# Kernel optimization log

Hardware: AMD Instinct MI355X
Metric: run time of the kernel (lower is better)

## Reference

```python
import jax, jax.numpy as jnp
import numpy as np

HEAD_SIZE = 64
EMBED_DIM = 1024
SEQ_LEN = 4096
BATCH = 4


def setup_inputs() -> dict:
    key = jax.random.key(0)
    kx, kk, kq, kv = jax.random.split(key, 4)
    x = jax.random.normal(kx, (BATCH, SEQ_LEN, EMBED_DIM), dtype=jnp.float32)
    # nn.Linear(embedding_dim, head_size, bias=False): weight [head_size, embed];
    # store transposed [embed, head_size] so projection is x @ W.
    scale = 1.0 / np.sqrt(EMBED_DIM)
    Wk = jax.random.uniform(kk, (EMBED_DIM, HEAD_SIZE), jnp.float32, -scale, scale)
    Wq = jax.random.uniform(kq, (EMBED_DIM, HEAD_SIZE), jnp.float32, -scale, scale)
    Wv = jax.random.uniform(kv, (EMBED_DIM, HEAD_SIZE), jnp.float32, -scale, scale)
    return {"x": x, "Wk": Wk, "Wq": Wq, "Wv": Wv}


def reference(x, Wk, Wq, Wv):
    B, T, C = x.shape
    k = x @ Wk  # [B, T, H]
    q = x @ Wq  # [B, T, H]
    v = x @ Wv  # [B, T, H]
    H = k.shape[-1]
    s = jnp.einsum('bth,bsh->bts', q, k) * (H ** -0.5)  # [B, T, T]
    causal = jnp.tril(jnp.ones((T, T), dtype=bool))
    s = jnp.where(causal, s, -jnp.inf)
    a = jax.nn.softmax(s, axis=-1)  # dropout p=0.0 -> identity
    z = jnp.einsum('bts,bsh->bth', a, v)  # [B, T, H]
    return z
```

## Files before the change

### kernel.cpp

```cpp
#include <hip/hip_runtime.h>

#define SEQ 4096
#define EMB 1024
#define HS 64

typedef __attribute__((ext_vector_type(8))) short bf16x8;
typedef __attribute__((ext_vector_type(4))) float f32x4;

__device__ __forceinline__ unsigned short f2b(float f) {
    union { float f; unsigned u; } v; v.f = f;
    unsigned r = v.u + 0x7fffu + ((v.u >> 16) & 1u);
    return (unsigned short)(r >> 16);
}
__device__ __forceinline__ float b2f(unsigned short h) {
    union { unsigned u; float f; } v; v.u = ((unsigned)h) << 16;
    return v.f;
}
template <typename T>
__device__ __forceinline__ void gll16(const T* g, void* l) {
    __builtin_amdgcn_global_load_lds(
        (const __attribute__((address_space(1))) unsigned int*)(g),
        (__attribute__((address_space(3))) unsigned int*)(l), 16, 0, 0);
}

__global__ __launch_bounds__(256) void wt_kernel(const float* __restrict__ Wq,
                                                 const float* __restrict__ Wk,
                                                 const float* __restrict__ Wv,
                                                 unsigned short* __restrict__ Wt) {
    int id = blockIdx.x * 256 + threadIdx.x;
    int mat = id >> 16;
    int rem = id & 65535;
    int k = rem >> 6;
    int n = rem & 63;
    const float* W = (mat == 0) ? Wq : (mat == 1) ? Wk : Wv;
    float scale = (mat == 0) ? 0.125f * 1.44269504f : 1.0f;
    Wt[(mat * HS + n) * EMB + k] = f2b(W[k * HS + n] * scale);
}

__global__ __launch_bounds__(256, 2) void proj_kernel(const float* __restrict__ x,
                                                      const unsigned short* __restrict__ Wt,
                                                      unsigned short* __restrict__ Qb,
                                                      unsigned short* __restrict__ Kb,
                                                      unsigned short* __restrict__ Vt) {
    __shared__ float xf[2][32 * 64];
    __shared__ unsigned short wb[2][192 * 64];
    const int tid = threadIdx.x;
    const int wave = tid >> 6, lane = tid & 63;
    const int col = lane & 15, quad = lane >> 4;
    const int m0 = blockIdx.x * 32;
    const int b = m0 >> 12, t0 = m0 & 4095;

    const int xr_in = lane >> 4;
    const int xc = lane & 15;
    const int wr_in = lane >> 3;
    const int wc = lane & 7;

    f32x4 acc[2][3];
    #pragma unroll
    for (int i = 0; i < 2; i++)
        #pragma unroll
        for (int j = 0; j < 3; j++) acc[i][j] = (f32x4){0.f, 0.f, 0.f, 0.f};

    auto stage = [&](int k0, int bufi) {
        #pragma unroll
        for (int t = 0; t < 2; t++) {
            int R = (wave + t * 4) * 4;
            int row = R + xr_in;
            gll16(x + (size_t)(m0 + row) * EMB + k0 + ((xc ^ (row & 15)) << 2),
                  &xf[bufi][R * 64]);
        }
        #pragma unroll
        for (int t = 0; t < 6; t++) {
            int R = (wave * 6 + t) * 8;
            int row = R + wr_in;
            gll16(Wt + (size_t)row * EMB + k0 + ((wc ^ (row & 7)) << 3),
                  &wb[bufi][R * 64]);
        }
    };

    stage(0, 0);
    int buf = 0;
    #pragma unroll 1
    for (int k0 = 0; k0 < EMB; k0 += 64) {
        __syncthreads();
        if (k0 + 64 < EMB) stage(k0 + 64, buf ^ 1);
        #pragma unroll
        for (int kc = 0; kc < 2; kc++) {
            const int q2 = quad + kc * 4;
            bf16x8 af[2], bfr[3];
            #pragma unroll
            for (int mt = 0; mt < 2; mt++) {
                int rr = mt * 16 + col;
                float4 lo = *(const float4*)&xf[buf][rr * 64 + (((2 * q2) ^ col) << 2)];
                float4 hi = *(const float4*)&xf[buf][rr * 64 + (((2 * q2 + 1) ^ col) << 2)];
                bf16x8 a;
                a[0] = (short)f2b(lo.x); a[1] = (short)f2b(lo.y);
                a[2] = (short)f2b(lo.z); a[3] = (short)f2b(lo.w);
                a[4] = (short)f2b(hi.x); a[5] = (short)f2b(hi.y);
                a[6] = (short)f2b(hi.z); a[7] = (short)f2b(hi.w);
                af[mt] = a;
            }
            #pragma unroll
            for (int nt = 0; nt < 3; nt++) {
                int rn = wave * 48 + nt * 16 + col;
                bfr[nt] = *(const bf16x8*)&wb[buf][rn * 64 + ((q2 ^ (col & 7)) << 3)];
            }
            #pragma unroll
            for (int mt = 0; mt < 2; mt++)
                #pragma unroll
                for (int nt = 0; nt < 3; nt++)
                    acc[mt][nt] = __builtin_amdgcn_mfma_f32_16x16x32_bf16(af[mt], bfr[nt], acc[mt][nt], 0, 0, 0);
        }
        buf ^= 1;
    }

    #pragma unroll
    for (int mt = 0; mt < 2; mt++)
        #pragma unroll
        for (int nt = 0; nt < 3; nt++) {
            const int g = wave * 3 + nt;
            const int mat = g >> 2;
            const int ncol = (g & 3) * 16 + col;
            #pragma unroll
            for (int r = 0; r < 4; r++) {
                unsigned short val = f2b(acc[mt][nt][r]);
                int row = mt * 16 + quad * 4 + r;
                if (mat == 0)      Qb[(size_t)(m0 + row) * HS + ncol] = val;
                else if (mat == 1) Kb[(size_t)(m0 + row) * HS + ncol] = val;
                else               Vt[((size_t)b * HS + ncol) * SEQ + t0 + row] = val;
            }
        }
}

__global__ __launch_bounds__(512, 4) void attn_kernel(const unsigned short* __restrict__ Qb,
                                                      const unsigned short* __restrict__ Kb,
                                                      const unsigned short* __restrict__ Vt,
                                                      unsigned short* __restrict__ Opart,
                                                      float* __restrict__ Lpart) {
    __shared__ unsigned short Kl[2][64 * 64];
    __shared__ unsigned short Vl[2][64 * 64];
    __shared__ unsigned short P_lds[8][16 * 72];
    const int tid = threadIdx.x;
    const int wave = tid >> 6, lane = tid & 63;
    const int col = lane & 15, quad = lane >> 4;
    const int bid = blockIdx.x;
    const int g = 101 - (bid >> 2);
    const int b = bid & 3;
    int T = 0, accp = 0;
    for (;;) { int np = (T + 6) / 6; if (accp + np > g) break; accp += np; T++; }
    const int piece = g - accp;
    const int q0 = T << 7;
    const int s_beg = piece * 12;
    const int s_end = min(s_beg + 12, 2 * T + 2);

    const unsigned short* Kp = Kb + ((size_t)(b << 12)) * HS;
    const unsigned short* Vp = Vt + (size_t)b * HS * SEQ;

    bf16x8 qf[2];
    #pragma unroll
    for (int c = 0; c < 2; c++)
        qf[c] = *(const bf16x8*)(Qb + ((size_t)(b << 12) + q0 + wave * 16 + col) * HS + quad * 8 + c * 32);

    f32x4 o[4];
    float l[4];
    #pragma unroll
    for (int ct = 0; ct < 4; ct++) o[ct] = (f32x4){0.f, 0.f, 0.f, 0.f};
    #pragma unroll
    for (int r = 0; r < 4; r++) l[r] = 0.f;

    const int r_in = lane >> 3;
    const int ch = lane & 7;

    auto stage = [&](int s, int bufi) {
        const int kv0 = s << 6;
        int R = wave * 8;
        int row = R + r_in;
        gll16(Kp + (size_t)(kv0 + row) * HS + ((ch ^ (row & 7)) << 3), &Kl[bufi][R * 64]);
        gll16(Vp + (size_t)row * SEQ + kv0 + ((ch ^ (row & 7)) << 3), &Vl[bufi][R * 64]);
    };

    stage(s_beg, 0);
    int buf = 0;
    const int rgb = q0 + wave * 16 + quad * 4;
    unsigned short* Pl = P_lds[wave];

    #pragma unroll 1
    for (int s = s_beg; s < s_end; s++) {
        __syncthreads();
        if (s + 1 < s_end) stage(s + 1, buf ^ 1);
        const int kv0 = s << 6;

        f32x4 sacc[4];
        #pragma unroll
        for (int ct = 0; ct < 4; ct++) sacc[ct] = (f32x4){0.f, 0.f, 0.f, 0.f};
        #pragma unroll
        for (int ct = 0; ct < 4; ct++) {
            int n = ct * 16 + col;
            #pragma unroll
            for (int kc = 0; kc < 2; kc++) {
                bf16x8 kf = *(const bf16x8*)&Kl[buf][n * 64 + (((kc * 4 + quad) ^ (col & 7)) << 3)];
                sacc[ct] = __builtin_amdgcn_mfma_f32_16x16x32_bf16(qf[kc], kf, sacc[ct], 0, 0, 0);
            }
        }

        float p[4][4];
        #pragma unroll
        for (int ct = 0; ct < 4; ct++) {
            int cg = kv0 + ct * 16 + col;
            #pragma unroll
            for (int r = 0; r < 4; r++) {
                float e = __builtin_exp2f(sacc[ct][r]);
                e = (cg > rgb + r) ? 0.f : e;
                p[ct][r] = e;
                l[r] += e;
            }
        }

        #pragma unroll
        for (int ct = 0; ct < 4; ct++)
            #pragma unroll
            for (int r = 0; r < 4; r++)
                Pl[(quad * 4 + r) * 72 + ct * 16 + col] = f2b(p[ct][r]);
        bf16x8 pf[2];
        #pragma unroll
        for (int c = 0; c < 2; c++)
            pf[c] = *(const bf16x8*)&Pl[col * 72 + quad * 8 + c * 32];

        #pragma unroll
        for (int ct = 0; ct < 4; ct++) {
            int h = ct * 16 + col;
            #pragma unroll
            for (int kc = 0; kc < 2; kc++) {
                bf16x8 vf = *(const bf16x8*)&Vl[buf][h * 64 + (((kc * 4 + quad) ^ (col & 7)) << 3)];
                o[ct] = __builtin_amdgcn_mfma_f32_16x16x32_bf16(pf[kc], vf, o[ct], 0, 0, 0);
            }
        }
        buf ^= 1;
    }

    #pragma unroll
    for (int off = 1; off < 16; off <<= 1)
        #pragma unroll
        for (int r = 0; r < 4; r++)
            l[r] += __shfl_xor(l[r], off, 64);

    const int widx = bid * 8 + wave;
    unsigned short* Op = Opart + (size_t)widx * 1024;
    #pragma unroll
    for (int ct = 0; ct < 4; ct++) {
        ushort4 st;
        st.x = f2b(o[ct][0]); st.y = f2b(o[ct][1]);
        st.z = f2b(o[ct][2]); st.w = f2b(o[ct][3]);
        *(ushort4*)(Op + ct * 256 + lane * 4) = st;
    }
    if (col == 0) {
        #pragma unroll
        for (int r = 0; r < 4; r++)
            Lpart[widx * 16 + quad * 4 + r] = l[r];
    }
}

__global__ __launch_bounds__(256) void comb_kernel(const unsigned short* __restrict__ Opart,
                                                   const float* __restrict__ Lpart,
                                                   float* __restrict__ out) {
    const int bid = blockIdx.x;
    const int b = bid & 3;
    const int T = (bid >> 2) & 31;
    const int wave = bid >> 7;
    const int tid = threadIdx.x;
    const int lane = tid & 63, ct = tid >> 6;
    const int col = lane & 15, quad = lane >> 4;

    const int q = T / 6, r6 = T % 6;
    const int base = (q + 1) * (3 * q + r6);
    const int np = (T + 6) / 6;

    float acc[4] = {0.f, 0.f, 0.f, 0.f};
    float l[4] = {0.f, 0.f, 0.f, 0.f};
    for (int p = 0; p < np; p++) {
        int gg = base + p;
        int bidp = ((101 - gg) << 2) | b;
        int widx = bidp * 8 + wave;
        ushort4 v = *(const ushort4*)(Opart + (size_t)widx * 1024 + ct * 256 + lane * 4);
        acc[0] += b2f(v.x); acc[1] += b2f(v.y);
        acc[2] += b2f(v.z); acc[3] += b2f(v.w);
        #pragma unroll
        for (int r = 0; r < 4; r++)
            l[r] += Lpart[widx * 16 + quad * 4 + r];
    }
    const size_t rowb = (size_t)(b << 12) + (T << 7) + wave * 16 + quad * 4;
    #pragma unroll
    for (int r = 0; r < 4; r++)
        out[(rowb + r) * HS + ct * 16 + col] = acc[r] / l[r];
}

extern "C" void kernel_launch(void* const* d_in, const int* in_sizes, int n_in,
                              void* d_out, int out_size, void* d_ws, size_t ws_size,
                              hipStream_t stream) {
    const float* x  = (const float*)d_in[0];
    const float* Wk = (const float*)d_in[1];
    const float* Wq = (const float*)d_in[2];
    const float* Wv = (const float*)d_in[3];
    float* out = (float*)d_out;

    char* ws = (char*)d_ws;
    unsigned short* Wt = (unsigned short*)(ws);
    unsigned short* Qb = (unsigned short*)(ws + 393216);
    unsigned short* Kb = (unsigned short*)(ws + 2490368);
    unsigned short* Vt = (unsigned short*)(ws + 4587520);
    unsigned short* Opart = (unsigned short*)(ws + 6684672);
    float* Lpart          = (float*)(ws + 13369344);

    wt_kernel<<<dim3(768), dim3(256), 0, stream>>>(Wq, Wk, Wv, Wt);
    proj_kernel<<<dim3(512), dim3(256), 0, stream>>>(x, Wt, Qb, Kb, Vt);
    attn_kernel<<<dim3(408), dim3(512), 0, stream>>>(Qb, Kb, Vt, Opart, Lpart);
    comb_kernel<<<dim3(1024), dim3(256), 0, stream>>>(Opart, Lpart, out);
}
```

Baseline: 152.8 us.

## Split projection output columns across two blocks to double grid size

The projection kernel now launches 1024 blocks, each computing half of the 192 fused Q/K/V output columns for a 32-row tile, with waves split by row half and column group. Shared memory for the weight tile is halved and the occupancy hint raised to 4 blocks per SM, so more blocks fit on the GPU's 256 CUs. The cost is that each x tile is loaded and converted to bf16 twice, once per column half, which doubles x traffic from global memory or L2.

```diff
diff --git a/kernel.cpp b/kernel.cpp
--- a/kernel.cpp
+++ b/kernel.cpp
@@ -37,29 +37,31 @@
     Wt[(mat * HS + n) * EMB + k] = f2b(W[k * HS + n] * scale);
 }
 
-__global__ __launch_bounds__(256, 2) void proj_kernel(const float* __restrict__ x,
+__global__ __launch_bounds__(256, 4) void proj_kernel(const float* __restrict__ x,
                                                       const unsigned short* __restrict__ Wt,
                                                       unsigned short* __restrict__ Qb,
                                                       unsigned short* __restrict__ Kb,
                                                       unsigned short* __restrict__ Vt) {
     __shared__ float xf[2][32 * 64];
-    __shared__ unsigned short wb[2][192 * 64];
+    __shared__ unsigned short wb[2][96 * 64];
     const int tid = threadIdx.x;
     const int wave = tid >> 6, lane = tid & 63;
     const int col = lane & 15, quad = lane >> 4;
-    const int m0 = blockIdx.x * 32;
+    const int bid = blockIdx.x;
+    const int cls = bid & 1;
+    const int m0 = (bid >> 1) * 32;
     const int b = m0 >> 12, t0 = m0 & 4095;
+    const int mh = wave & 1;
+    const int ngrp = wave >> 1;
 
     const int xr_in = lane >> 4;
     const int xc = lane & 15;
     const int wr_in = lane >> 3;
     const int wc = lane & 7;
 
-    f32x4 acc[2][3];
-    #pragma unroll
-    for (int i = 0; i < 2; i++)
-        #pragma unroll
-        for (int j = 0; j < 3; j++) acc[i][j] = (f32x4){0.f, 0.f, 0.f, 0.f};
+    f32x4 acc[3];
+    #pragma unroll
+    for (int j = 0; j < 3; j++) acc[j] = (f32x4){0.f, 0.f, 0.f, 0.f};
 
     auto stage = [&](int k0, int bufi) {
         #pragma unroll
@@ -70,10 +72,10 @@
                   &xf[bufi][R * 64]);
         }
         #pragma unroll
-        for (int t = 0; t < 6; t++) {
-            int R = (wave * 6 + t) * 8;
+        for (int t = 0; t < 3; t++) {
+            int R = (wave * 3 + t) * 8;
             int row = R + wr_in;
-            gll16(Wt + (size_t)row * EMB + k0 + ((wc ^ (row & 7)) << 3),
+            gll16(Wt + (size_t)(cls * 96 + row) * EMB + k0 + ((wc ^ (row & 7)) << 3),
                   &wb[bufi][R * 64]);
         }
     };
@@ -87,49 +89,38 @@
         #pragma unroll
         for (int kc = 0; kc < 2; kc++) {
             const int q2 = quad + kc * 4;
-            bf16x8 af[2], bfr[3];
-            #pragma unroll
-            for (int mt = 0; mt < 2; mt++) {
-                int rr = mt * 16 + col;
-                float4 lo = *(const float4*)&xf[buf][rr * 64 + (((2 * q2) ^ col) << 2)];
-                float4 hi = *(const float4*)&xf[buf][rr * 64 + (((2 * q2 + 1) ^ col) << 2)];
-                bf16x8 a;
-                a[0] = (short)f2b(lo.x); a[1] = (short)f2b(lo.y);
-                a[2] = (short)f2b(lo.z); a[3] = (short)f2b(lo.w);
-                a[4] = (short)f2b(hi.x); a[5] = (short)f2b(hi.y);
-                a[6] = (short)f2b(hi.z); a[7] = (short)f2b(hi.w);
-                af[mt] = a;
+            const int rr = mh * 16 + col;
+            float4 lo = *(const float4*)&xf[buf][rr * 64 + (((2 * q2) ^ col) << 2)];
+            float4 hi = *(const float4*)&xf[buf][rr * 64 + (((2 * q2 + 1) ^ col) << 2)];
+            bf16x8 af;
+            af[0] = (short)f2b(lo.x); af[1] = (short)f2b(lo.y);
+            af[2] = (short)f2b(lo.z); af[3] = (short)f2b(lo.w);
+            af[4] = (short)f2b(hi.x); af[5] = (short)f2b(hi.y);
+            af[6] = (short)f2b(hi.z); af[7] = (short)f2b(hi.w);
+            #pragma unroll
+            for (int nt = 0; nt < 3; nt++) {
+                int rn = ngrp * 48 + nt * 16 + col;
+                bf16x8 bfr = *(const bf16x8*)&wb[buf][rn * 64 + ((q2 ^ (col & 7)) << 3)];
+                acc[nt] = __builtin_amdgcn_mfma_f32_16x16x32_bf16(af, bfr, acc[nt], 0, 0, 0);
             }
-            #pragma unroll
-            for (int nt = 0; nt < 3; nt++) {
-                int rn = wave * 48 + nt * 16 + col;
-                bfr[nt] = *(const bf16x8*)&wb[buf][rn * 64 + ((q2 ^ (col & 7)) << 3)];
-            }
-            #pragma unroll
-            for (int mt = 0; mt < 2; mt++)
-                #pragma unroll
-                for (int nt = 0; nt < 3; nt++)
-                    acc[mt][nt] = __builtin_amdgcn_mfma_f32_16x16x32_bf16(af[mt], bfr[nt], acc[mt][nt], 0, 0, 0);
         }
         buf ^= 1;
     }
 
     #pragma unroll
-    for (int mt = 0; mt < 2; mt++)
-        #pragma unroll
-        for (int nt = 0; nt < 3; nt++) {
-            const int g = wave * 3 + nt;
-            const int mat = g >> 2;
-            const int ncol = (g & 3) * 16 + col;
-            #pragma unroll
-            for (int r = 0; r < 4; r++) {
-                unsigned short val = f2b(acc[mt][nt][r]);
-                int row = mt * 16 + quad * 4 + r;
-                if (mat == 0)      Qb[(size_t)(m0 + row) * HS + ncol] = val;
-                else if (mat == 1) Kb[(size_t)(m0 + row) * HS + ncol] = val;
-                else               Vt[((size_t)b * HS + ncol) * SEQ + t0 + row] = val;
-            }
-        }
+    for (int nt = 0; nt < 3; nt++) {
+        const int G = cls * 96 + ngrp * 48 + nt * 16 + col;
+        const int mat = G >> 6;
+        const int nc = G & 63;
+        #pragma unroll
+        for (int r = 0; r < 4; r++) {
+            unsigned short val = f2b(acc[nt][r]);
+            int row = mh * 16 + quad * 4 + r;
+            if (mat == 0)      Qb[(size_t)(m0 + row) * HS + nc] = val;
+            else if (mat == 1) Kb[(size_t)(m0 + row) * HS + nc] = val;
+            else               Vt[((size_t)b * HS + nc) * SEQ + t0 + row] = val;
+        }
+    }
 }
 
 __global__ __launch_bounds__(512, 4) void attn_kernel(const unsigned short* __restrict__ Qb,
@@ -312,7 +303,7 @@
     float* Lpart          = (float*)(ws + 13369344);
 
     wt_kernel<<<dim3(768), dim3(256), 0, stream>>>(Wq, Wk, Wv, Wt);
-    proj_kernel<<<dim3(512), dim3(256), 0, stream>>>(x, Wt, Qb, Kb, Vt);
+    proj_kernel<<<dim3(1024), dim3(256), 0, stream>>>(x, Wt, Qb, Kb, Vt);
     attn_kernel<<<dim3(408), dim3(512), 0, stream>>>(Qb, Kb, Vt, Opart, Lpart);
     comb_kernel<<<dim3(1024), dim3(256), 0, stream>>>(Opart, Lpart, out);
 }
```

New measurement: 155.8 us. Within noise of the previous version (+2.0%).

## Fuse split-KV combine into attention kernel via atomic last-arriver counters

Applied to the files above, without the earlier changes.

Removes the separate combine kernel launch. Each attention wave writes its partial output and row sums, then increments a per-(batch, tile, wave) counter with an atomic. The last-arriving wave reads all partials and writes the final normalized output. The counters are zeroed in the weight-transpose kernel. This saves a kernel launch and its tail, at the cost of fences, atomics, and extra work in the tail waves.

```diff
diff --git a/kernel.cpp b/kernel.cpp
--- a/kernel.cpp
+++ b/kernel.cpp
@@ -26,8 +26,10 @@
 __global__ __launch_bounds__(256) void wt_kernel(const float* __restrict__ Wq,
                                                  const float* __restrict__ Wk,
                                                  const float* __restrict__ Wv,
-                                                 unsigned short* __restrict__ Wt) {
+                                                 unsigned short* __restrict__ Wt,
+                                                 unsigned int* __restrict__ cnt) {
     int id = blockIdx.x * 256 + threadIdx.x;
+    if (id < 1024) cnt[id] = 0u;
     int mat = id >> 16;
     int rem = id & 65535;
     int k = rem >> 6;
@@ -136,7 +138,9 @@
                                                       const unsigned short* __restrict__ Kb,
                                                       const unsigned short* __restrict__ Vt,
                                                       unsigned short* __restrict__ Opart,
-                                                      float* __restrict__ Lpart) {
+                                                      float* __restrict__ Lpart,
+                                                      unsigned int* __restrict__ cnt,
+                                                      float* __restrict__ out) {
     __shared__ unsigned short Kl[2][64 * 64];
     __shared__ unsigned short Vl[2][64 * 64];
     __shared__ unsigned short P_lds[8][16 * 72];
@@ -149,6 +153,8 @@
     int T = 0, accp = 0;
     for (;;) { int np = (T + 6) / 6; if (accp + np > g) break; accp += np; T++; }
     const int piece = g - accp;
+    const int np = (T + 6) / 6;
+    const int base = accp;
     const int q0 = T << 7;
     const int s_beg = piece * 12;
     const int s_end = min(s_beg + 12, 2 * T + 2);
@@ -181,6 +187,7 @@
 
     stage(s_beg, 0);
     int buf = 0;
+    const int grb = (b << 12) + q0 + wave * 16;
     const int rgb = q0 + wave * 16 + quad * 4;
     unsigned short* Pl = P_lds[wave];
 
@@ -258,40 +265,44 @@
         for (int r = 0; r < 4; r++)
             Lpart[widx * 16 + quad * 4 + r] = l[r];
     }
-}
-
-__global__ __launch_bounds__(256) void comb_kernel(const unsigned short* __restrict__ Opart,
-                                                   const float* __restrict__ Lpart,
-                                                   float* __restrict__ out) {
-    const int bid = blockIdx.x;
-    const int b = bid & 3;
-    const int T = (bid >> 2) & 31;
-    const int wave = bid >> 7;
-    const int tid = threadIdx.x;
-    const int lane = tid & 63, ct = tid >> 6;
-    const int col = lane & 15, quad = lane >> 4;
-
-    const int q = T / 6, r6 = T % 6;
-    const int base = (q + 1) * (3 * q + r6);
-    const int np = (T + 6) / 6;
-
-    float acc[4] = {0.f, 0.f, 0.f, 0.f};
-    float l[4] = {0.f, 0.f, 0.f, 0.f};
-    for (int p = 0; p < np; p++) {
-        int gg = base + p;
-        int bidp = ((101 - gg) << 2) | b;
-        int widx = bidp * 8 + wave;
-        ushort4 v = *(const ushort4*)(Opart + (size_t)widx * 1024 + ct * 256 + lane * 4);
-        acc[0] += b2f(v.x); acc[1] += b2f(v.y);
-        acc[2] += b2f(v.z); acc[3] += b2f(v.w);
-        #pragma unroll
-        for (int r = 0; r < 4; r++)
-            l[r] += Lpart[widx * 16 + quad * 4 + r];
-    }
-    const size_t rowb = (size_t)(b << 12) + (T << 7) + wave * 16 + quad * 4;
-    #pragma unroll
-    for (int r = 0; r < 4; r++)
-        out[(rowb + r) * HS + ct * 16 + col] = acc[r] / l[r];
+
+    __threadfence();
+    const int ci = ((b << 5) + T) * 8 + wave;
+    unsigned int old = 0;
+    if (lane == 0)
+        old = __hip_atomic_fetch_add(&cnt[ci], 1u, __ATOMIC_ACQ_REL, __HIP_MEMORY_SCOPE_AGENT);
+    old = (unsigned int)__shfl((int)old, 0, 64);
+    if (old == (unsigned int)(np - 1)) {
+        __threadfence();
+        float acc[4][4], lsum[4] = {0.f, 0.f, 0.f, 0.f};
+        #pragma unroll
+        for (int ct = 0; ct < 4; ct++)
+            #pragma unroll
+            for (int e = 0; e < 4; e++) acc[ct][e] = 0.f;
+        for (int p = 0; p < np; p++) {
+            int bidp = ((101 - (base + p)) << 2) | b;
+            int wp = bidp * 8 + wave;
+            #pragma unroll
+            for (int ct = 0; ct < 4; ct++) {
+                unsigned long long u = __hip_atomic_load(
+                    (const unsigned long long*)(Opart + (size_t)wp * 1024 + ct * 256 + lane * 4),
+                    __ATOMIC_RELAXED, __HIP_MEMORY_SCOPE_AGENT);
+                acc[ct][0] += b2f((unsigned short)(u));
+                acc[ct][1] += b2f((unsigned short)(u >> 16));
+                acc[ct][2] += b2f((unsigned short)(u >> 32));
+                acc[ct][3] += b2f((unsigned short)(u >> 48));
+            }
+            #pragma unroll
+            for (int e = 0; e < 4; e++)
+                lsum[e] += __hip_atomic_load(&Lpart[wp * 16 + quad * 4 + e],
+                                             __ATOMIC_RELAXED, __HIP_MEMORY_SCOPE_AGENT);
+        }
+        #pragma unroll
+        for (int ct = 0; ct < 4; ct++)
+            #pragma unroll
+            for (int e = 0; e < 4; e++)
+                out[(size_t)(grb + quad * 4 + e) * HS + ct * 16 + col] = acc[ct][e] / lsum[e];
+    }
 }
 
 extern "C" void kernel_launch(void* const* d_in, const int* in_sizes, int n_in,
@@ -310,9 +321,9 @@
     unsigned short* Vt = (unsigned short*)(ws + 4587520);
     unsigned short* Opart = (unsigned short*)(ws + 6684672);
     float* Lpart          = (float*)(ws + 13369344);
-
-    wt_kernel<<<dim3(768), dim3(256), 0, stream>>>(Wq, Wk, Wv, Wt);
+    unsigned int* cnt     = (unsigned int*)(ws + 13578240);
+
+    wt_kernel<<<dim3(768), dim3(256), 0, stream>>>(Wq, Wk, Wv, Wt, cnt);
     proj_kernel<<<dim3(512), dim3(256), 0, stream>>>(x, Wt, Qb, Kb, Vt);
-    attn_kernel<<<dim3(408), dim3(512), 0, stream>>>(Qb, Kb, Vt, Opart, Lpart);
-    comb_kernel<<<dim3(1024), dim3(256), 0, stream>>>(Opart, Lpart, out);
-}
+    attn_kernel<<<dim3(408), dim3(512), 0, stream>>>(Qb, Kb, Vt, Opart, Lpart, cnt, out);
+}
```

Result: slower. 294.8 us (+93.0%).
